# Kernel tuning notes

Measured on AMD Instinct MI355X. Metric: run time of the kernel, lower is better.

The kernel has to match this reference:

```python
import jax, jax.numpy as jnp
import numpy as np

DIM = 768
NUM_HEADS = 12
HEAD_DIM = DIM // NUM_HEADS  # 64
H = W = 48


def setup_inputs() -> dict:
    key = jax.random.key(0)
    ks = jax.random.split(key, 7)
    x = jax.random.normal(ks[0], (2, H, W, DIM), dtype=jnp.float32)
    # qkv Linear: stored as [in, out] for x @ W convention
    qkv_w = jax.random.normal(ks[1], (DIM, 3 * DIM), dtype=jnp.float32) * (DIM ** -0.5)
    qkv_b = jax.random.normal(ks[2], (3 * DIM,), dtype=jnp.float32) * 0.02
    proj_w = jax.random.normal(ks[3], (DIM, DIM), dtype=jnp.float32) * (DIM ** -0.5)
    proj_b = jax.random.normal(ks[4], (DIM,), dtype=jnp.float32) * 0.02
    # decomposed relative position tables (trunc_normal std=0.02 ~ normal*0.02)
    rel_pos_h = jax.random.normal(ks[5], (2 * H - 1, HEAD_DIM), dtype=jnp.float32) * 0.02
    rel_pos_w = jax.random.normal(ks[6], (2 * W - 1, HEAD_DIM), dtype=jnp.float32) * 0.02
    return {"x": x, "qkv_w": qkv_w, "qkv_b": qkv_b, "proj_w": proj_w,
            "proj_b": proj_b, "rel_pos_h": rel_pos_h, "rel_pos_w": rel_pos_w}


def _get_rel_pos(size, rel_pos):
    # q_size == k_size == size; table already has 2*size-1 entries, no interp
    coords = jnp.arange(size)[:, None] - jnp.arange(size)[None, :] + (size - 1)
    return rel_pos[coords]  # [size, size, head_dim]


def reference(x, qkv_w, qkv_b, proj_w, proj_b, rel_pos_h, rel_pos_w):
    B, h, w, dim = x.shape
    nh, hd = NUM_HEADS, HEAD_DIM
    S = h * w
    scale = hd ** -0.5
    qkv = (x.reshape(B, S, dim) @ qkv_w + qkv_b).reshape(B, S, 3, nh, hd)
    qkv = jnp.transpose(qkv, (2, 0, 3, 1, 4)).reshape(3, B * nh, S, hd)
    q, k, v = qkv[0], qkv[1], qkv[2]
    attn = jnp.einsum("bqc,bkc->bqk", q * scale, k)  # [B*nh, S, S]
    # decomposed relative position bias
    Rh = _get_rel_pos(h, rel_pos_h)  # [h, h, hd]
    Rw = _get_rel_pos(w, rel_pos_w)  # [w, w, hd]
    r_q = q.reshape(B * nh, h, w, hd)
    rel_h = jnp.einsum("bhwc,hkc->bhwk", r_q, Rh)  # [B*nh, h, w, h]
    rel_w = jnp.einsum("bhwc,wkc->bhwk", r_q, Rw)  # [B*nh, h, w, w]
    attn = (attn.reshape(B * nh, h, w, h, w)
            + rel_h[:, :, :, :, None]
            + rel_w[:, :, :, None, :]).reshape(B * nh, S, S)
    attn = jax.nn.softmax(attn, axis=-1)
    out = (attn @ v).reshape(B, nh, h, w, hd)
    out = jnp.transpose(out, (0, 2, 3, 1, 4)).reshape(B, h, w, dim)
    return out @ proj_w + proj_b
```

## Files before the change

kernel.cpp:

```cpp
#include <hip/hip_runtime.h>
#include <hip/hip_fp16.h>

#define HD 64
#define SEQ 2304

typedef unsigned short u16;
typedef unsigned int u32;
using f32x4 = __attribute__((ext_vector_type(4))) float;
using s16x8 = __attribute__((ext_vector_type(8))) short;

static __device__ __forceinline__ u16 f2bf(float x) {
  union { float f; u32 u; } a; a.f = x;
  u32 r = a.u + 0x7fffu + ((a.u >> 16) & 1u);
  return (u16)(r >> 16);
}
static __device__ __forceinline__ float bf2f(u16 h) {
  union { float f; u32 u; } a; a.u = ((u32)h) << 16; return a.f;
}

__global__ __launch_bounds__(256) void conv_wT_k(
    const float* __restrict__ src, u16* __restrict__ dhi, u16* __restrict__ dlo,
    int K, int N)
{
  __shared__ u32 t[64][65];
  const int tid = threadIdx.x;
  const int n0 = blockIdx.x * 64, k0 = blockIdx.y * 64;
  const int r = tid >> 2, c0 = (tid & 3) * 16;
  const float* sp = src + (size_t)(k0 + r) * N + n0 + c0;
#pragma unroll
  for (int j = 0; j < 16; j += 4) {
    f32x4 v = *(const f32x4*)(sp + j);
#pragma unroll
    for (int e = 0; e < 4; e++) {
      float x = v[e];
      u16 h = f2bf(x);
      u16 l = f2bf(x - bf2f(h));
      t[r][c0 + j + e] = (u32)h | ((u32)l << 16);
    }
  }
  __syncthreads();
  u16 hb[16], lb[16];
#pragma unroll
  for (int j = 0; j < 16; j++) {
    u32 p = t[c0 + j][r];
    hb[j] = (u16)(p & 0xffffu);
    lb[j] = (u16)(p >> 16);
  }
  size_t off = (size_t)(n0 + r) * K + k0 + c0;
  *(uint4*)(dhi + off)     = *(uint4*)&hb[0];
  *(uint4*)(dhi + off + 8) = *(uint4*)&hb[8];
  *(uint4*)(dlo + off)     = *(uint4*)&lb[0];
  *(uint4*)(dlo + off + 8) = *(uint4*)&lb[8];
}

__global__ __launch_bounds__(256) void qkv_mfma_k(
    const float* __restrict__ x, const u16* __restrict__ bthi, const u16* __restrict__ btlo,
    const float* __restrict__ bias,
    float* __restrict__ qbuf, u16* __restrict__ khi, u16* __restrict__ klo,
    u16* __restrict__ vhi, u16* __restrict__ vlo)
{
  __shared__ __align__(16) u16 Ah[128*40], Al[128*40], Bh2[128*40], Bl2[128*40];
  const int tid = threadIdx.x;
  const int lane = tid & 63, wid = tid >> 6;
  const int g = lane >> 4, ql = lane & 15;
  const int wr = wid >> 1, wc = wid & 1;
  const int c0 = blockIdx.x * 128, r0 = blockIdx.y * 128;
  const int srow = tid >> 1, half = tid & 1;

  const float* ag = x + (size_t)(r0 + srow) * 768 + half * 16;
  const u16* bgh = bthi + (size_t)(c0 + srow) * 768 + half * 16;
  const u16* bgl = btlo + (size_t)(c0 + srow) * 768 + half * 16;

  f32x4 pa[4]; uint4 pbh[2], pbl[2];
#pragma unroll
  for (int j = 0; j < 4; j++) pa[j] = *(const f32x4*)(ag + j * 4);
  pbh[0] = *(const uint4*)bgh; pbh[1] = *(const uint4*)(bgh + 8);
  pbl[0] = *(const uint4*)bgl; pbl[1] = *(const uint4*)(bgl + 8);

  f32x4 acc[4][4] = {};

  for (int ks = 0; ks < 24; ks++) {
    __syncthreads();
    {
      u16 hb[16], lb[16];
#pragma unroll
      for (int j = 0; j < 16; j++) {
        float xv = pa[j >> 2][j & 3];
        u16 h = f2bf(xv);
        hb[j] = h; lb[j] = f2bf(xv - bf2f(h));
      }
      u16* d1 = Ah + srow * 40 + half * 16;
      u16* d2 = Al + srow * 40 + half * 16;
      *(uint4*)d1 = *(uint4*)&hb[0];
      *(uint4*)(d1 + 8) = *(uint4*)&hb[8];
      *(uint4*)d2 = *(uint4*)&lb[0];
      *(uint4*)(d2 + 8) = *(uint4*)&lb[8];
      u16* d3 = Bh2 + srow * 40 + half * 16;
      u16* d4 = Bl2 + srow * 40 + half * 16;
      *(uint4*)d3 = pbh[0]; *(uint4*)(d3 + 8) = pbh[1];
      *(uint4*)d4 = pbl[0]; *(uint4*)(d4 + 8) = pbl[1];
    }
    __syncthreads();
    if (ks < 23) {
      const float* a2 = ag + (ks + 1) * 32;
#pragma unroll
      for (int j = 0; j < 4; j++) pa[j] = *(const f32x4*)(a2 + j * 4);
      pbh[0] = *(const uint4*)(bgh + (ks + 1) * 32);
      pbh[1] = *(const uint4*)(bgh + (ks + 1) * 32 + 8);
      pbl[0] = *(const uint4*)(bgl + (ks + 1) * 32);
      pbl[1] = *(const uint4*)(bgl + (ks + 1) * 32 + 8);
    }
    s16x8 bfh[4], bfl[4];
#pragma unroll
    for (int nt = 0; nt < 4; nt++) {
      bfh[nt] = *(const s16x8*)(Bh2 + (wc * 64 + nt * 16 + ql) * 40 + g * 8);
      bfl[nt] = *(const s16x8*)(Bl2 + (wc * 64 + nt * 16 + ql) * 40 + g * 8);
    }
#pragma unroll
    for (int mt = 0; mt < 4; mt++) {
      s16x8 ah = *(const s16x8*)(Ah + (wr * 64 + mt * 16 + ql) * 40 + g * 8);
      s16x8 al = *(const s16x8*)(Al + (wr * 64 + mt * 16 + ql) * 40 + g * 8);
#pragma unroll
      for (int nt = 0; nt < 4; nt++) {
        acc[mt][nt] = __builtin_amdgcn_mfma_f32_16x16x32_bf16(ah, bfh[nt], acc[mt][nt], 0, 0, 0);
        acc[mt][nt] = __builtin_amdgcn_mfma_f32_16x16x32_bf16(ah, bfl[nt], acc[mt][nt], 0, 0, 0);
        acc[mt][nt] = __builtin_amdgcn_mfma_f32_16x16x32_bf16(al, bfh[nt], acc[mt][nt], 0, 0, 0);
      }
    }
  }
  const int col0 = c0 + wc * 64;
  const int row0 = r0 + wr * 64;
  const int hb36 = col0 >> 6;
  const int which = hb36 / 12, head = hb36 - (hb36 / 12) * 12;
  const int b = row0 / 2304;
  const int sb = row0 - b * 2304;
  const int bh = b * 12 + head;
  float bb[4];
#pragma unroll
  for (int nt = 0; nt < 4; nt++) bb[nt] = bias[col0 + nt * 16 + ql];
  if (which == 0) {
#pragma unroll
    for (int mt = 0; mt < 4; mt++)
#pragma unroll
      for (int nt = 0; nt < 4; nt++)
#pragma unroll
        for (int r = 0; r < 4; r++) {
          int s = sb + mt * 16 + g * 4 + r;
          qbuf[((size_t)bh * SEQ + s) * 64 + nt * 16 + ql] = acc[mt][nt][r] + bb[nt];
        }
  } else {
    const int kt = sb >> 6;
    const size_t tile = ((size_t)bh * 36 + kt) * 4096;
    if (which == 1) {
#pragma unroll
      for (int mt = 0; mt < 4; mt++)
#pragma unroll
        for (int nt = 0; nt < 4; nt++) {
          int pc = (nt >> 1) * 32 + (ql >> 2) * 8 + (nt & 1) * 4 + (ql & 3);
#pragma unroll
          for (int r = 0; r < 4; r++) {
            int key = mt * 16 + g * 4 + r;
            float xv = acc[mt][nt][r] + bb[nt];
            u16 h = f2bf(xv);
            khi[tile + key * 64 + pc] = h;
            klo[tile + key * 64 + pc] = f2bf(xv - bf2f(h));
          }
        }
    } else {
#pragma unroll
      for (int mt = 0; mt < 4; mt++)
#pragma unroll
        for (int nt = 0; nt < 4; nt++)
#pragma unroll
          for (int r = 0; r < 4; r++) {
            int d = nt * 16 + ql;
            int vc = (mt >> 1) * 32 + g * 8 + (mt & 1) * 4 + r;
            float xv = acc[mt][nt][r] + bb[nt];
            u16 h = f2bf(xv);
            vhi[tile + d * 64 + vc] = h;
            vlo[tile + d * 64 + vc] = f2bf(xv - bf2f(h));
          }
    }
  }
}

__global__ __launch_bounds__(512) void attn_k(
    const float* __restrict__ qb,
    const u16* __restrict__ khi, const u16* __restrict__ klo,
    const u16* __restrict__ vhi, const u16* __restrict__ vlo,
    const float* __restrict__ rph, const float* __restrict__ rpw,
    float* __restrict__ ao)
{
  __shared__ __align__(16) char pool[49664];
  u16* KhiL = (u16*)pool;
  u16* KloL = (u16*)(pool + 9216);
  u16* VhL  = (u16*)(pool + 18432);
  u16* VlL  = (u16*)(pool + 27648);
  __half* Bh = (__half*)(pool + 36864);
  __half* Bw = (__half*)(pool + 43008);
  float* m_s = (float*)(pool + 49152);
  float* l_s = (float*)(pool + 49408);
  float* qlds = (float*)pool;
  float* o_s  = (float*)pool;

  const int tid  = threadIdx.x;
  const int lane = tid & 63;
  const int wid  = tid >> 6;
  const int g    = lane >> 4;
  const int ql   = lane & 15;
  const int wq   = wid & 3;
  const int hh   = wid >> 2;
  const int qt   = blockIdx.x;
  const int bh   = blockIdx.y;
  const int s0   = qt * 64;

  {
    int row = tid >> 3, c0 = (tid & 7) * 8;
    const float* src = qb + ((size_t)bh * SEQ + s0 + row) * HD + c0;
    f32x4 v0 = *(const f32x4*)src;
    f32x4 v1 = *(const f32x4*)(src + 4);
    *(f32x4*)&qlds[row * 68 + c0]     = v0;
    *(f32x4*)&qlds[row * 68 + c0 + 4] = v1;
  }
  __syncthreads();

  s16x8 qfh[2], qfl[2];
  {
    int qrow = wq * 16 + ql;
#pragma unroll
    for (int ds = 0; ds < 2; ds++) {
#pragma unroll
      for (int h2 = 0; h2 < 2; h2++) {
        f32x4 qv = *(const f32x4*)&qlds[qrow * 68 + g * 4 + h2 * 16 + ds * 32];
#pragma unroll
        for (int j = 0; j < 4; j++) {
          float xx = qv[j];
          u16 hi = f2bf(xx);
          u16 lo = f2bf(xx - bf2f(hi));
          qfh[ds][h2 * 4 + j] = (short)hi;
          qfl[ds][h2 * 4 + j] = (short)lo;
        }
      }
    }
  }

  const size_t tbK = (size_t)bh * 36 * 4096;
  const int srow = tid >> 3;
  const int sch  = ((tid & 7) - (srow & 7)) & 7;
  const size_t soff = (size_t)srow * 64 + sch * 8;
  uint4 rkh = *(const uint4*)(khi + tbK + soff);
  uint4 rkl = *(const uint4*)(klo + tbK + soff);
  uint4 rvh = *(const uint4*)(vhi + tbK + soff);
  uint4 rvl = *(const uint4*)(vlo + tbK + soff);

  for (int i = tid; i < 64 * 96; i += 512) {
    int q = i / 96, j = i - (i / 96) * 96;
    int s = s0 + q;
    int qhg = s / 48, qw = s - qhg * 48;
    const float* tab;
    int ridx, col;
    if (j < 48) { col = j;      ridx = qhg - j + 47;        tab = rph; }
    else        { col = j - 48; ridx = qw - (j - 48) + 47;  tab = rpw; }
    const float* rp = tab + (size_t)ridx * HD;
    const float* qp = &qlds[q * 68];
    float s1 = 0.f;
#pragma unroll 4
    for (int d = 0; d < 64; d += 4) {
      f32x4 a = *(const f32x4*)(qp + d);
      f32x4 bv = *(const f32x4*)(rp + d);
      s1 += a[0]*bv[0] + a[1]*bv[1] + a[2]*bv[2] + a[3]*bv[3];
    }
    if (j < 48) Bh[col * 64 + q] = __float2half_rn(s1);
    else        Bw[col * 64 + q] = __float2half_rn(s1);
  }

  float m_r = -3.0e38f, l_r = 0.f;
  f32x4 oacc[4] = {};
  const int q64b = wq * 16 + ql;

  for (int kt = 0; kt < 36; kt++) {
    __syncthreads();
    *(uint4*)(KhiL + srow * 72 + sch * 8) = rkh;
    *(uint4*)(KloL + srow * 72 + sch * 8) = rkl;
    *(uint4*)(VhL  + srow * 72 + sch * 8) = rvh;
    *(uint4*)(VlL  + srow * 72 + sch * 8) = rvl;
    __syncthreads();
    if (kt < 35) {
      size_t tb = tbK + (size_t)(kt + 1) * 4096;
      rkh = *(const uint4*)(khi + tb + soff);
      rkl = *(const uint4*)(klo + tb + soff);
      rvh = *(const uint4*)(vhi + tb + soff);
      rvl = *(const uint4*)(vlo + tb + soff);
    }

    f32x4 sacc[2] = {};
#pragma unroll
    for (int ds = 0; ds < 2; ds++) {
#pragma unroll
      for (int t2 = 0; t2 < 2; t2++) {
        int row = (hh * 2 + t2) * 16 + ql;
        s16x8 af = *(const s16x8*)(KhiL + row * 72 + ds * 32 + g * 8);
        s16x8 al = *(const s16x8*)(KloL + row * 72 + ds * 32 + g * 8);
        sacc[t2] = __builtin_amdgcn_mfma_f32_16x16x32_bf16(af, qfh[ds], sacc[t2], 0, 0, 0);
        sacc[t2] = __builtin_amdgcn_mfma_f32_16x16x32_bf16(af, qfl[ds], sacc[t2], 0, 0, 0);
        sacc[t2] = __builtin_amdgcn_mfma_f32_16x16x32_bf16(al, qfh[ds], sacc[t2], 0, 0, 0);
      }
    }

    float lg[8];
    float tmax = -3.0e38f;
#pragma unroll
    for (int t2 = 0; t2 < 2; t2++)
#pragma unroll
      for (int r = 0; r < 4; r++) {
        u32 kg = (u32)(kt * 64 + hh * 32 + t2 * 16 + g * 4 + r);
        u32 kh = kg / 48u;
        u32 kw = kg - kh * 48u;
        float x = sacc[t2][r] * 0.125f
                + __half2float(Bh[(int)kh * 64 + q64b])
                + __half2float(Bw[(int)kw * 64 + q64b]);
        lg[t2 * 4 + r] = x;
        tmax = fmaxf(tmax, x);
      }
    tmax = fmaxf(tmax, __shfl_xor(tmax, 16));
    tmax = fmaxf(tmax, __shfl_xor(tmax, 32));
    if (__any(tmax > m_r + 6.0f)) {
      float mnew = fmaxf(m_r, tmax);
      float corr = __expf(m_r - mnew);
      l_r *= corr;
      m_r = mnew;
      float cq[4];
#pragma unroll
      for (int r = 0; r < 4; r++) cq[r] = __shfl(corr, g * 4 + r);
#pragma unroll
      for (int dt = 0; dt < 4; dt++)
#pragma unroll
        for (int r = 0; r < 4; r++) oacc[dt][r] *= cq[r];
    }
    float psum = 0.f;
    s16x8 pfh, pfl;
#pragma unroll
    for (int j = 0; j < 8; j++) {
      float p = __expf(lg[j] - m_r);
      psum += p;
      u16 hi = f2bf(p);
      pfh[j] = (short)hi;
      pfl[j] = (short)f2bf(p - bf2f(hi));
    }
    psum += __shfl_xor(psum, 16);
    psum += __shfl_xor(psum, 32);
    l_r += psum;

#pragma unroll
    for (int dt = 0; dt < 4; dt++) {
      int row = ql + 16 * dt;
      s16x8 bhf = *(const s16x8*)(VhL + row * 72 + hh * 32 + g * 8);
      s16x8 blf = *(const s16x8*)(VlL + row * 72 + hh * 32 + g * 8);
      oacc[dt] = __builtin_amdgcn_mfma_f32_16x16x32_bf16(pfh, bhf, oacc[dt], 0, 0, 0);
      oacc[dt] = __builtin_amdgcn_mfma_f32_16x16x32_bf16(pfh, blf, oacc[dt], 0, 0, 0);
      oacc[dt] = __builtin_amdgcn_mfma_f32_16x16x32_bf16(pfl, bhf, oacc[dt], 0, 0, 0);
    }
  }

  __syncthreads();
  if (hh == 1) {
    if (g == 0) { m_s[wq * 16 + ql] = m_r; l_s[wq * 16 + ql] = l_r; }
#pragma unroll
    for (int dt = 0; dt < 4; dt++)
#pragma unroll
      for (int r = 0; r < 4; r++)
        o_s[(wq * 16 + g * 4 + r) * 68 + ql + 16 * dt] = oacc[dt][r];
  }
  __syncthreads();
  if (hh == 0) {
    float m2 = m_s[wq * 16 + ql];
    float l2 = l_s[wq * 16 + ql];
    float mf = fmaxf(m_r, m2);
    float c1 = __expf(m_r - mf);
    float c2 = __expf(m2 - mf);
    float lf = l_r * c1 + l2 * c2;
    float c1q[4], c2q[4], lfq[4];
#pragma unroll
    for (int r = 0; r < 4; r++) {
      c1q[r] = __shfl(c1, g * 4 + r);
      c2q[r] = __shfl(c2, g * 4 + r);
      lfq[r] = __shfl(lf, g * 4 + r);
    }
    const int b = bh / 12, head = bh - (bh / 12) * 12;
#pragma unroll
    for (int dt = 0; dt < 4; dt++)
#pragma unroll
      for (int r = 0; r < 4; r++) {
        float oo = oacc[dt][r] * c1q[r]
                 + o_s[(wq * 16 + g * 4 + r) * 68 + ql + 16 * dt] * c2q[r];
        int s = s0 + wq * 16 + g * 4 + r;
        ao[((size_t)b * SEQ + s) * 768 + head * 64 + ql + 16 * dt] = oo / lfq[r];
      }
  }
}

__global__ __launch_bounds__(256) void proj_mfma_k(
    const float* __restrict__ a, const u16* __restrict__ bthi, const u16* __restrict__ btlo,
    const float* __restrict__ bias, float* __restrict__ out)
{
  __shared__ __align__(16) u16 Ah[128*40], Al[128*40], Bh2[128*40], Bl2[128*40];
  const int tid = threadIdx.x;
  const int lane = tid & 63, wid = tid >> 6;
  const int g = lane >> 4, ql = lane & 15;
  const int wr = wid >> 1, wc = wid & 1;
  const int c0 = blockIdx.x * 128, r0 = blockIdx.y * 128;
  const int srow = tid >> 1, half = tid & 1;

  const float* ag = a + (size_t)(r0 + srow) * 768 + half * 16;
  const u16* bgh = bthi + (size_t)(c0 + srow) * 768 + half * 16;
  const u16* bgl = btlo + (size_t)(c0 + srow) * 768 + half * 16;

  f32x4 pa[4]; uint4 pbh[2], pbl[2];
#pragma unroll
  for (int j = 0; j < 4; j++) pa[j] = *(const f32x4*)(ag + j * 4);
  pbh[0] = *(const uint4*)bgh; pbh[1] = *(const uint4*)(bgh + 8);
  pbl[0] = *(const uint4*)bgl; pbl[1] = *(const uint4*)(bgl + 8);

  f32x4 acc[4][4] = {};

  for (int ks = 0; ks < 24; ks++) {
    __syncthreads();
    {
      u16 hb[16], lb[16];
#pragma unroll
      for (int j = 0; j < 16; j++) {
        float xv = pa[j >> 2][j & 3];
        u16 h = f2bf(xv);
        hb[j] = h; lb[j] = f2bf(xv - bf2f(h));
      }
      u16* d1 = Ah + srow * 40 + half * 16;
      u16* d2 = Al + srow * 40 + half * 16;
      *(uint4*)d1 = *(uint4*)&hb[0];
      *(uint4*)(d1 + 8) = *(uint4*)&hb[8];
      *(uint4*)d2 = *(uint4*)&lb[0];
      *(uint4*)(d2 + 8) = *(uint4*)&lb[8];
      u16* d3 = Bh2 + srow * 40 + half * 16;
      u16* d4 = Bl2 + srow * 40 + half * 16;
      *(uint4*)d3 = pbh[0]; *(uint4*)(d3 + 8) = pbh[1];
      *(uint4*)d4 = pbl[0]; *(uint4*)(d4 + 8) = pbl[1];
    }
    __syncthreads();
    if (ks < 23) {
      const float* a2 = ag + (ks + 1) * 32;
#pragma unroll
      for (int j = 0; j < 4; j++) pa[j] = *(const f32x4*)(a2 + j * 4);
      pbh[0] = *(const uint4*)(bgh + (ks + 1) * 32);
      pbh[1] = *(const uint4*)(bgh + (ks + 1) * 32 + 8);
      pbl[0] = *(const uint4*)(bgl + (ks + 1) * 32);
      pbl[1] = *(const uint4*)(bgl + (ks + 1) * 32 + 8);
    }
    s16x8 bfh[4], bfl[4];
#pragma unroll
    for (int nt = 0; nt < 4; nt++) {
      bfh[nt] = *(const s16x8*)(Bh2 + (wc * 64 + nt * 16 + ql) * 40 + g * 8);
      bfl[nt] = *(const s16x8*)(Bl2 + (wc * 64 + nt * 16 + ql) * 40 + g * 8);
    }
#pragma unroll
    for (int mt = 0; mt < 4; mt++) {
      s16x8 ah = *(const s16x8*)(Ah + (wr * 64 + mt * 16 + ql) * 40 + g * 8);
      s16x8 al = *(const s16x8*)(Al + (wr * 64 + mt * 16 + ql) * 40 + g * 8);
#pragma unroll
      for (int nt = 0; nt < 4; nt++) {
        acc[mt][nt] = __builtin_amdgcn_mfma_f32_16x16x32_bf16(ah, bfh[nt], acc[mt][nt], 0, 0, 0);
        acc[mt][nt] = __builtin_amdgcn_mfma_f32_16x16x32_bf16(ah, bfl[nt], acc[mt][nt], 0, 0, 0);
        acc[mt][nt] = __builtin_amdgcn_mfma_f32_16x16x32_bf16(al, bfh[nt], acc[mt][nt], 0, 0, 0);
      }
    }
  }
  const int col0 = c0 + wc * 64;
  const int row0 = r0 + wr * 64;
  float bb[4];
#pragma unroll
  for (int nt = 0; nt < 4; nt++) bb[nt] = bias[col0 + nt * 16 + ql];
#pragma unroll
  for (int mt = 0; mt < 4; mt++)
#pragma unroll
    for (int nt = 0; nt < 4; nt++)
#pragma unroll
      for (int r = 0; r < 4; r++)
        out[(size_t)(row0 + mt * 16 + g * 4 + r) * 768 + col0 + nt * 16 + ql] =
            acc[mt][nt][r] + bb[nt];
}

extern "C" void kernel_launch(void* const* d_in, const int* in_sizes, int n_in,
                              void* d_out, int out_size, void* d_ws, size_t ws_size,
                              hipStream_t stream) {
  const float* x      = (const float*)d_in[0];
  const float* qkv_w  = (const float*)d_in[1];
  const float* qkv_b  = (const float*)d_in[2];
  const float* proj_w = (const float*)d_in[3];
  const float* proj_b = (const float*)d_in[4];
  const float* rph    = (const float*)d_in[5];
  const float* rpw    = (const float*)d_in[6];
  float* out = (float*)d_out;
  float* ws  = (float*)d_ws;

  const size_t SZ = (size_t)24 * SEQ * HD;
  float* qbuf = ws;
  u16* khi = (u16*)(ws + SZ);
  u16* klo = khi + SZ;
  u16* vhi = klo + SZ;
  u16* vlo = vhi + SZ;
  float* ao = ws + 3 * SZ;
  u16* wqThi = (u16*)(ws + 4 * SZ);
  u16* wqTlo = wqThi + 768 * 2304;
  u16* wpThi = wqTlo + 768 * 2304;
  u16* wpTlo = wpThi + 768 * 768;

  conv_wT_k <<<dim3(36, 12), 256, 0, stream>>>(qkv_w, wqThi, wqTlo, 768, 2304);
  conv_wT_k <<<dim3(12, 12), 256, 0, stream>>>(proj_w, wpThi, wpTlo, 768, 768);
  qkv_mfma_k<<<dim3(18, 36), 256, 0, stream>>>(x, wqThi, wqTlo, qkv_b,
                                               qbuf, khi, klo, vhi, vlo);
  attn_k    <<<dim3(36, 24), 512, 0, stream>>>(qbuf, khi, klo, vhi, vlo, rph, rpw, ao);
  proj_mfma_k<<<dim3(6, 36), 256, 0, stream>>>(ao, wpThi, wpTlo, proj_b, out);
}
```

Measured before the change: 522.1 us.

## Load K/V fragments directly from global memory, dropping LDS staging and barriers

Each wave now reads its K and V MFMA fragments straight from global memory (likely L2-resident) into registers instead of staging whole tiles through LDS with two barriers per iteration. This removes per-iteration __syncthreads and LDS traffic and shrinks shared memory, which can raise occupancy. It also pads the relative-position bias tables to stride 68 and wraps the MFMA sections in s_setprio. The cost is that global loads now sit on the critical path with no explicit prefetch, and K/V data is fetched redundantly by the waves that share it.

```diff
diff --git a/kernel.cpp b/kernel.cpp
--- a/kernel.cpp
+++ b/kernel.cpp
@@ -191,17 +191,13 @@
     const float* __restrict__ rph, const float* __restrict__ rpw,
     float* __restrict__ ao)
 {
-  __shared__ __align__(16) char pool[49664];
-  u16* KhiL = (u16*)pool;
-  u16* KloL = (u16*)(pool + 9216);
-  u16* VhL  = (u16*)(pool + 18432);
-  u16* VlL  = (u16*)(pool + 27648);
-  __half* Bh = (__half*)(pool + 36864);
-  __half* Bw = (__half*)(pool + 43008);
-  float* m_s = (float*)(pool + 49152);
-  float* l_s = (float*)(pool + 49408);
+  __shared__ __align__(16) char pool[30976];
   float* qlds = (float*)pool;
   float* o_s  = (float*)pool;
+  __half* Bh = (__half*)(pool + 17408);
+  __half* Bw = (__half*)(pool + 23936);
+  float* m_s = (float*)(pool + 30464);
+  float* l_s = (float*)(pool + 30720);
 
   const int tid  = threadIdx.x;
   const int lane = tid & 63;
@@ -243,15 +239,6 @@
       }
     }
   }
-
-  const size_t tbK = (size_t)bh * 36 * 4096;
-  const int srow = tid >> 3;
-  const int sch  = ((tid & 7) - (srow & 7)) & 7;
-  const size_t soff = (size_t)srow * 64 + sch * 8;
-  uint4 rkh = *(const uint4*)(khi + tbK + soff);
-  uint4 rkl = *(const uint4*)(klo + tbK + soff);
-  uint4 rvh = *(const uint4*)(vhi + tbK + soff);
-  uint4 rvl = *(const uint4*)(vlo + tbK + soff);
 
   for (int i = tid; i < 64 * 96; i += 512) {
     int q = i / 96, j = i - (i / 96) * 96;
@@ -270,42 +257,51 @@
       f32x4 bv = *(const f32x4*)(rp + d);
       s1 += a[0]*bv[0] + a[1]*bv[1] + a[2]*bv[2] + a[3]*bv[3];
     }
-    if (j < 48) Bh[col * 64 + q] = __float2half_rn(s1);
-    else        Bw[col * 64 + q] = __float2half_rn(s1);
-  }
+    if (j < 48) Bh[col * 68 + q] = __float2half_rn(s1);
+    else        Bw[col * 68 + q] = __float2half_rn(s1);
+  }
+  __syncthreads();
 
   float m_r = -3.0e38f, l_r = 0.f;
   f32x4 oacc[4] = {};
   const int q64b = wq * 16 + ql;
+  const size_t tbK = (size_t)bh * 36 * 4096;
+
+  const int koff0 = ((hh * 2 + 0) * 16 + ql) * 64 + g * 8;
+  const int koff1 = ((hh * 2 + 1) * 16 + ql) * 64 + g * 8;
+  const int voffb = ql * 64 + hh * 32 + g * 8;
 
   for (int kt = 0; kt < 36; kt++) {
-    __syncthreads();
-    *(uint4*)(KhiL + srow * 72 + sch * 8) = rkh;
-    *(uint4*)(KloL + srow * 72 + sch * 8) = rkl;
-    *(uint4*)(VhL  + srow * 72 + sch * 8) = rvh;
-    *(uint4*)(VlL  + srow * 72 + sch * 8) = rvl;
-    __syncthreads();
-    if (kt < 35) {
-      size_t tb = tbK + (size_t)(kt + 1) * 4096;
-      rkh = *(const uint4*)(khi + tb + soff);
-      rkl = *(const uint4*)(klo + tb + soff);
-      rvh = *(const uint4*)(vhi + tb + soff);
-      rvl = *(const uint4*)(vlo + tb + soff);
+    const size_t tb = tbK + (size_t)kt * 4096;
+    const u16* Kh = khi + tb; const u16* Kl = klo + tb;
+    const u16* Vh = vhi + tb; const u16* Vl = vlo + tb;
+
+    s16x8 af[2][2], al[2][2], bhf[4], blf[4];
+#pragma unroll
+    for (int ds = 0; ds < 2; ds++) {
+      af[ds][0] = *(const s16x8*)(Kh + koff0 + ds * 32);
+      af[ds][1] = *(const s16x8*)(Kh + koff1 + ds * 32);
+      al[ds][0] = *(const s16x8*)(Kl + koff0 + ds * 32);
+      al[ds][1] = *(const s16x8*)(Kl + koff1 + ds * 32);
+    }
+#pragma unroll
+    for (int dt = 0; dt < 4; dt++) {
+      bhf[dt] = *(const s16x8*)(Vh + voffb + dt * 1024);
+      blf[dt] = *(const s16x8*)(Vl + voffb + dt * 1024);
     }
 
     f32x4 sacc[2] = {};
+    __builtin_amdgcn_s_setprio(1);
 #pragma unroll
     for (int ds = 0; ds < 2; ds++) {
 #pragma unroll
       for (int t2 = 0; t2 < 2; t2++) {
-        int row = (hh * 2 + t2) * 16 + ql;
-        s16x8 af = *(const s16x8*)(KhiL + row * 72 + ds * 32 + g * 8);
-        s16x8 al = *(const s16x8*)(KloL + row * 72 + ds * 32 + g * 8);
-        sacc[t2] = __builtin_amdgcn_mfma_f32_16x16x32_bf16(af, qfh[ds], sacc[t2], 0, 0, 0);
-        sacc[t2] = __builtin_amdgcn_mfma_f32_16x16x32_bf16(af, qfl[ds], sacc[t2], 0, 0, 0);
-        sacc[t2] = __builtin_amdgcn_mfma_f32_16x16x32_bf16(al, qfh[ds], sacc[t2], 0, 0, 0);
-      }
-    }
+        sacc[t2] = __builtin_amdgcn_mfma_f32_16x16x32_bf16(af[ds][t2], qfh[ds], sacc[t2], 0, 0, 0);
+        sacc[t2] = __builtin_amdgcn_mfma_f32_16x16x32_bf16(af[ds][t2], qfl[ds], sacc[t2], 0, 0, 0);
+        sacc[t2] = __builtin_amdgcn_mfma_f32_16x16x32_bf16(al[ds][t2], qfh[ds], sacc[t2], 0, 0, 0);
+      }
+    }
+    __builtin_amdgcn_s_setprio(0);
 
     float lg[8];
     float tmax = -3.0e38f;
@@ -317,8 +313,8 @@
         u32 kh = kg / 48u;
         u32 kw = kg - kh * 48u;
         float x = sacc[t2][r] * 0.125f
-                + __half2float(Bh[(int)kh * 64 + q64b])
-                + __half2float(Bw[(int)kw * 64 + q64b]);
+                + __half2float(Bh[(int)kh * 68 + q64b])
+                + __half2float(Bw[(int)kw * 68 + q64b]);
         lg[t2 * 4 + r] = x;
         tmax = fmaxf(tmax, x);
       }
@@ -351,15 +347,14 @@
     psum += __shfl_xor(psum, 32);
     l_r += psum;
 
+    __builtin_amdgcn_s_setprio(1);
 #pragma unroll
     for (int dt = 0; dt < 4; dt++) {
-      int row = ql + 16 * dt;
-      s16x8 bhf = *(const s16x8*)(VhL + row * 72 + hh * 32 + g * 8);
-      s16x8 blf = *(const s16x8*)(VlL + row * 72 + hh * 32 + g * 8);
-      oacc[dt] = __builtin_amdgcn_mfma_f32_16x16x32_bf16(pfh, bhf, oacc[dt], 0, 0, 0);
-      oacc[dt] = __builtin_amdgcn_mfma_f32_16x16x32_bf16(pfh, blf, oacc[dt], 0, 0, 0);
-      oacc[dt] = __builtin_amdgcn_mfma_f32_16x16x32_bf16(pfl, bhf, oacc[dt], 0, 0, 0);
-    }
+      oacc[dt] = __builtin_amdgcn_mfma_f32_16x16x32_bf16(pfh, bhf[dt], oacc[dt], 0, 0, 0);
+      oacc[dt] = __builtin_amdgcn_mfma_f32_16x16x32_bf16(pfh, blf[dt], oacc[dt], 0, 0, 0);
+      oacc[dt] = __builtin_amdgcn_mfma_f32_16x16x32_bf16(pfl, bhf[dt], oacc[dt], 0, 0, 0);
+    }
+    __builtin_amdgcn_s_setprio(0);
   }
 
   __syncthreads();
```

Measured after the change: 900.0 us. +72.4%, slower.

## Process 128 queries per attention block to reuse K/V tiles across two query subtiles

Applied to the files above, without the earlier changes.

Each attention block now handles 128 query rows instead of 64, so every wave carries two 16-row query subtiles against each staged K/V tile. Each K/V tile is loaded from global memory and LDS once and used for twice as many MFMAs, halving K/V traffic. The grid is reordered so blocks for the same head sit next to each other, and s_setprio is raised around the MFMA sections. In exchange the block has half as many blocks (432), needs more registers and a larger LDS pool, and launch_bounds requests 4 waves per EU, which may cause spills.

```diff
diff --git a/kernel.cpp b/kernel.cpp
--- a/kernel.cpp
+++ b/kernel.cpp
@@ -184,22 +184,22 @@
   }
 }
 
-__global__ __launch_bounds__(512) void attn_k(
+__global__ __launch_bounds__(512, 4) void attn_k(
     const float* __restrict__ qb,
     const u16* __restrict__ khi, const u16* __restrict__ klo,
     const u16* __restrict__ vhi, const u16* __restrict__ vlo,
     const float* __restrict__ rph, const float* __restrict__ rpw,
     float* __restrict__ ao)
 {
-  __shared__ __align__(16) char pool[49664];
+  __shared__ __align__(16) char pool[63232];
   u16* KhiL = (u16*)pool;
   u16* KloL = (u16*)(pool + 9216);
   u16* VhL  = (u16*)(pool + 18432);
   u16* VlL  = (u16*)(pool + 27648);
   __half* Bh = (__half*)(pool + 36864);
-  __half* Bw = (__half*)(pool + 43008);
-  float* m_s = (float*)(pool + 49152);
-  float* l_s = (float*)(pool + 49408);
+  __half* Bw = (__half*)(pool + 49536);
+  float* m_s = (float*)(pool + 62208);
+  float* l_s = (float*)(pool + 62720);
   float* qlds = (float*)pool;
   float* o_s  = (float*)pool;
 
@@ -208,25 +208,25 @@
   const int wid  = tid >> 6;
   const int g    = lane >> 4;
   const int ql   = lane & 15;
-  const int wq   = wid & 3;
+  const int wqq  = wid & 3;
   const int hh   = wid >> 2;
-  const int qt   = blockIdx.x;
-  const int bh   = blockIdx.y;
-  const int s0   = qt * 64;
+  const int bh   = blockIdx.x;
+  const int qt   = blockIdx.y;
+  const int s0   = qt * 128;
 
   {
-    int row = tid >> 3, c0 = (tid & 7) * 8;
+    int row = tid >> 2, c0 = (tid & 3) * 16;
     const float* src = qb + ((size_t)bh * SEQ + s0 + row) * HD + c0;
-    f32x4 v0 = *(const f32x4*)src;
-    f32x4 v1 = *(const f32x4*)(src + 4);
-    *(f32x4*)&qlds[row * 68 + c0]     = v0;
-    *(f32x4*)&qlds[row * 68 + c0 + 4] = v1;
+#pragma unroll
+    for (int j = 0; j < 16; j += 4)
+      *(f32x4*)&qlds[row * 68 + c0 + j] = *(const f32x4*)(src + j);
   }
   __syncthreads();
 
-  s16x8 qfh[2], qfl[2];
-  {
-    int qrow = wq * 16 + ql;
+  s16x8 qfh[2][2], qfl[2][2];
+#pragma unroll
+  for (int qs = 0; qs < 2; qs++) {
+    int qrow = wqq * 32 + qs * 16 + ql;
 #pragma unroll
     for (int ds = 0; ds < 2; ds++) {
 #pragma unroll
@@ -237,8 +237,8 @@
           float xx = qv[j];
           u16 hi = f2bf(xx);
           u16 lo = f2bf(xx - bf2f(hi));
-          qfh[ds][h2 * 4 + j] = (short)hi;
-          qfl[ds][h2 * 4 + j] = (short)lo;
+          qfh[qs][ds][h2 * 4 + j] = (short)hi;
+          qfl[qs][ds][h2 * 4 + j] = (short)lo;
         }
       }
     }
@@ -253,7 +253,7 @@
   uint4 rvh = *(const uint4*)(vhi + tbK + soff);
   uint4 rvl = *(const uint4*)(vlo + tbK + soff);
 
-  for (int i = tid; i < 64 * 96; i += 512) {
+  for (int i = tid; i < 128 * 96; i += 512) {
     int q = i / 96, j = i - (i / 96) * 96;
     int s = s0 + q;
     int qhg = s / 48, qw = s - qhg * 48;
@@ -270,13 +270,13 @@
       f32x4 bv = *(const f32x4*)(rp + d);
       s1 += a[0]*bv[0] + a[1]*bv[1] + a[2]*bv[2] + a[3]*bv[3];
     }
-    if (j < 48) Bh[col * 64 + q] = __float2half_rn(s1);
-    else        Bw[col * 64 + q] = __float2half_rn(s1);
-  }
-
-  float m_r = -3.0e38f, l_r = 0.f;
-  f32x4 oacc[4] = {};
-  const int q64b = wq * 16 + ql;
+    if (j < 48) Bh[col * 132 + q] = __float2half_rn(s1);
+    else        Bw[col * 132 + q] = __float2half_rn(s1);
+  }
+
+  float m_r[2] = {-3.0e38f, -3.0e38f};
+  float l_r[2] = {0.f, 0.f};
+  f32x4 oacc[2][4] = {};
 
   for (int kt = 0; kt < 36; kt++) {
     __syncthreads();
@@ -293,7 +293,8 @@
       rvl = *(const uint4*)(vlo + tb + soff);
     }
 
-    f32x4 sacc[2] = {};
+    f32x4 sacc[2][2] = {};
+    __builtin_amdgcn_s_setprio(1);
 #pragma unroll
     for (int ds = 0; ds < 2; ds++) {
 #pragma unroll
@@ -301,101 +302,124 @@
         int row = (hh * 2 + t2) * 16 + ql;
         s16x8 af = *(const s16x8*)(KhiL + row * 72 + ds * 32 + g * 8);
         s16x8 al = *(const s16x8*)(KloL + row * 72 + ds * 32 + g * 8);
-        sacc[t2] = __builtin_amdgcn_mfma_f32_16x16x32_bf16(af, qfh[ds], sacc[t2], 0, 0, 0);
-        sacc[t2] = __builtin_amdgcn_mfma_f32_16x16x32_bf16(af, qfl[ds], sacc[t2], 0, 0, 0);
-        sacc[t2] = __builtin_amdgcn_mfma_f32_16x16x32_bf16(al, qfh[ds], sacc[t2], 0, 0, 0);
-      }
-    }
-
-    float lg[8];
-    float tmax = -3.0e38f;
-#pragma unroll
-    for (int t2 = 0; t2 < 2; t2++)
-#pragma unroll
-      for (int r = 0; r < 4; r++) {
-        u32 kg = (u32)(kt * 64 + hh * 32 + t2 * 16 + g * 4 + r);
-        u32 kh = kg / 48u;
-        u32 kw = kg - kh * 48u;
-        float x = sacc[t2][r] * 0.125f
-                + __half2float(Bh[(int)kh * 64 + q64b])
-                + __half2float(Bw[(int)kw * 64 + q64b]);
-        lg[t2 * 4 + r] = x;
-        tmax = fmaxf(tmax, x);
-      }
-    tmax = fmaxf(tmax, __shfl_xor(tmax, 16));
-    tmax = fmaxf(tmax, __shfl_xor(tmax, 32));
-    if (__any(tmax > m_r + 6.0f)) {
-      float mnew = fmaxf(m_r, tmax);
-      float corr = __expf(m_r - mnew);
-      l_r *= corr;
-      m_r = mnew;
-      float cq[4];
-#pragma unroll
-      for (int r = 0; r < 4; r++) cq[r] = __shfl(corr, g * 4 + r);
-#pragma unroll
-      for (int dt = 0; dt < 4; dt++)
-#pragma unroll
-        for (int r = 0; r < 4; r++) oacc[dt][r] *= cq[r];
-    }
-    float psum = 0.f;
-    s16x8 pfh, pfl;
-#pragma unroll
-    for (int j = 0; j < 8; j++) {
-      float p = __expf(lg[j] - m_r);
-      psum += p;
-      u16 hi = f2bf(p);
-      pfh[j] = (short)hi;
-      pfl[j] = (short)f2bf(p - bf2f(hi));
-    }
-    psum += __shfl_xor(psum, 16);
-    psum += __shfl_xor(psum, 32);
-    l_r += psum;
-
+#pragma unroll
+        for (int qs = 0; qs < 2; qs++) {
+          sacc[t2][qs] = __builtin_amdgcn_mfma_f32_16x16x32_bf16(af, qfh[qs][ds], sacc[t2][qs], 0, 0, 0);
+          sacc[t2][qs] = __builtin_amdgcn_mfma_f32_16x16x32_bf16(af, qfl[qs][ds], sacc[t2][qs], 0, 0, 0);
+          sacc[t2][qs] = __builtin_amdgcn_mfma_f32_16x16x32_bf16(al, qfh[qs][ds], sacc[t2][qs], 0, 0, 0);
+        }
+      }
+    }
+    __builtin_amdgcn_s_setprio(0);
+
+    s16x8 pfh[2], pfl[2];
+#pragma unroll
+    for (int qs = 0; qs < 2; qs++) {
+      const int q128 = wqq * 32 + qs * 16 + ql;
+      float lg[8];
+      float tmax = -3.0e38f;
+#pragma unroll
+      for (int t2 = 0; t2 < 2; t2++)
+#pragma unroll
+        for (int r = 0; r < 4; r++) {
+          u32 kg = (u32)(kt * 64 + hh * 32 + t2 * 16 + g * 4 + r);
+          u32 kh = kg / 48u;
+          u32 kw = kg - kh * 48u;
+          float x = sacc[t2][qs][r] * 0.125f
+                  + __half2float(Bh[(int)kh * 132 + q128])
+                  + __half2float(Bw[(int)kw * 132 + q128]);
+          lg[t2 * 4 + r] = x;
+          tmax = fmaxf(tmax, x);
+        }
+      tmax = fmaxf(tmax, __shfl_xor(tmax, 16));
+      tmax = fmaxf(tmax, __shfl_xor(tmax, 32));
+      if (__any(tmax > m_r[qs] + 6.0f)) {
+        float mnew = fmaxf(m_r[qs], tmax);
+        float corr = __expf(m_r[qs] - mnew);
+        l_r[qs] *= corr;
+        m_r[qs] = mnew;
+        float cq[4];
+#pragma unroll
+        for (int r = 0; r < 4; r++) cq[r] = __shfl(corr, g * 4 + r);
+#pragma unroll
+        for (int dt = 0; dt < 4; dt++)
+#pragma unroll
+          for (int r = 0; r < 4; r++) oacc[qs][dt][r] *= cq[r];
+      }
+      float psum = 0.f;
+#pragma unroll
+      for (int j = 0; j < 8; j++) {
+        float p = __expf(lg[j] - m_r[qs]);
+        psum += p;
+        u16 hi = f2bf(p);
+        pfh[qs][j] = (short)hi;
+        pfl[qs][j] = (short)f2bf(p - bf2f(hi));
+      }
+      psum += __shfl_xor(psum, 16);
+      psum += __shfl_xor(psum, 32);
+      l_r[qs] += psum;
+    }
+
+    __builtin_amdgcn_s_setprio(1);
 #pragma unroll
     for (int dt = 0; dt < 4; dt++) {
       int row = ql + 16 * dt;
       s16x8 bhf = *(const s16x8*)(VhL + row * 72 + hh * 32 + g * 8);
       s16x8 blf = *(const s16x8*)(VlL + row * 72 + hh * 32 + g * 8);
-      oacc[dt] = __builtin_amdgcn_mfma_f32_16x16x32_bf16(pfh, bhf, oacc[dt], 0, 0, 0);
-      oacc[dt] = __builtin_amdgcn_mfma_f32_16x16x32_bf16(pfh, blf, oacc[dt], 0, 0, 0);
-      oacc[dt] = __builtin_amdgcn_mfma_f32_16x16x32_bf16(pfl, bhf, oacc[dt], 0, 0, 0);
-    }
+#pragma unroll
+      for (int qs = 0; qs < 2; qs++) {
+        oacc[qs][dt] = __builtin_amdgcn_mfma_f32_16x16x32_bf16(pfh[qs], bhf, oacc[qs][dt], 0, 0, 0);
+        oacc[qs][dt] = __builtin_amdgcn_mfma_f32_16x16x32_bf16(pfh[qs], blf, oacc[qs][dt], 0, 0, 0);
+        oacc[qs][dt] = __builtin_amdgcn_mfma_f32_16x16x32_bf16(pfl[qs], bhf, oacc[qs][dt], 0, 0, 0);
+      }
+    }
+    __builtin_amdgcn_s_setprio(0);
   }
 
   __syncthreads();
   if (hh == 1) {
-    if (g == 0) { m_s[wq * 16 + ql] = m_r; l_s[wq * 16 + ql] = l_r; }
-#pragma unroll
-    for (int dt = 0; dt < 4; dt++)
-#pragma unroll
-      for (int r = 0; r < 4; r++)
-        o_s[(wq * 16 + g * 4 + r) * 68 + ql + 16 * dt] = oacc[dt][r];
+#pragma unroll
+    for (int qs = 0; qs < 2; qs++) {
+      if (g == 0) {
+        m_s[wqq * 32 + qs * 16 + ql] = m_r[qs];
+        l_s[wqq * 32 + qs * 16 + ql] = l_r[qs];
+      }
+#pragma unroll
+      for (int dt = 0; dt < 4; dt++)
+#pragma unroll
+        for (int r = 0; r < 4; r++)
+          o_s[(wqq * 32 + qs * 16 + g * 4 + r) * 68 + ql + 16 * dt] = oacc[qs][dt][r];
+    }
   }
   __syncthreads();
   if (hh == 0) {
-    float m2 = m_s[wq * 16 + ql];
-    float l2 = l_s[wq * 16 + ql];
-    float mf = fmaxf(m_r, m2);
-    float c1 = __expf(m_r - mf);
-    float c2 = __expf(m2 - mf);
-    float lf = l_r * c1 + l2 * c2;
-    float c1q[4], c2q[4], lfq[4];
-#pragma unroll
-    for (int r = 0; r < 4; r++) {
-      c1q[r] = __shfl(c1, g * 4 + r);
-      c2q[r] = __shfl(c2, g * 4 + r);
-      lfq[r] = __shfl(lf, g * 4 + r);
-    }
     const int b = bh / 12, head = bh - (bh / 12) * 12;
 #pragma unroll
-    for (int dt = 0; dt < 4; dt++)
+    for (int qs = 0; qs < 2; qs++) {
+      const int q128 = wqq * 32 + qs * 16 + ql;
+      float m2 = m_s[q128];
+      float l2 = l_s[q128];
+      float mf = fmaxf(m_r[qs], m2);
+      float c1 = __expf(m_r[qs] - mf);
+      float c2 = __expf(m2 - mf);
+      float lf = l_r[qs] * c1 + l2 * c2;
+      float c1q[4], c2q[4], lfq[4];
 #pragma unroll
       for (int r = 0; r < 4; r++) {
-        float oo = oacc[dt][r] * c1q[r]
-                 + o_s[(wq * 16 + g * 4 + r) * 68 + ql + 16 * dt] * c2q[r];
-        int s = s0 + wq * 16 + g * 4 + r;
-        ao[((size_t)b * SEQ + s) * 768 + head * 64 + ql + 16 * dt] = oo / lfq[r];
-      }
+        c1q[r] = __shfl(c1, g * 4 + r);
+        c2q[r] = __shfl(c2, g * 4 + r);
+        lfq[r] = __shfl(lf, g * 4 + r);
+      }
+#pragma unroll
+      for (int dt = 0; dt < 4; dt++)
+#pragma unroll
+        for (int r = 0; r < 4; r++) {
+          float oo = oacc[qs][dt][r] * c1q[r]
+                   + o_s[(wqq * 32 + qs * 16 + g * 4 + r) * 68 + ql + 16 * dt] * c2q[r];
+          int s = s0 + wqq * 32 + qs * 16 + g * 4 + r;
+          ao[((size_t)b * SEQ + s) * 768 + head * 64 + ql + 16 * dt] = oo / lfq[r];
+        }
+    }
   }
 }
 
@@ -516,6 +540,6 @@
   conv_wT_k <<<dim3(12, 12), 256, 0, stream>>>(proj_w, wpThi, wpTlo, 768, 768);
   qkv_mfma_k<<<dim3(18, 36), 256, 0, stream>>>(x, wqThi, wqTlo, qkv_b,
                                                qbuf, khi, klo, vhi, vlo);
-  attn_k    <<<dim3(36, 24), 512, 0, stream>>>(qbuf, khi, klo, vhi, vlo, rph, rpw, ao);
+  attn_k    <<<dim3(24, 18), 512, 0, stream>>>(qbuf, khi, klo, vhi, vlo, rph, rpw, ao);
   proj_mfma_k<<<dim3(6, 36), 256, 0, stream>>>(ao, wpThi, wpTlo, proj_b, out);
 }
```

Measured after the change: 555.8 us. 1.06x slower.
